# Optimization experiments

Measured on AMD Instinct MI355X. Metric: run time of the kernel, lower is better.

The kernel has to match this reference:

```python
import jax, jax.numpy as jnp
import numpy as np

N = 512
C = 64
B = 1048576


def setup_inputs() -> dict:
    key = jax.random.key(0)
    k1, k2, k3, k4 = jax.random.split(key, 4)
    coords = jax.random.uniform(k1, (B, 3), dtype=jnp.float32, minval=-0.5, maxval=0.5)
    x_line = jax.random.normal(k2, (N, C), dtype=jnp.float32)
    y_line = jax.random.normal(k3, (N, C), dtype=jnp.float32)
    z_line = jax.random.normal(k4, (N, C), dtype=jnp.float32)
    grid = jnp.linspace(-0.5, 0.5, N, dtype=jnp.float32)
    return {"coords": coords, "x_line": x_line, "y_line": y_line, "z_line": z_line, "grid": grid}


def _interp_1d(line_feat, coord, grid):
    # line_feat: [N, C], coord: [B] in [-0.5, 0.5]
    n = line_feat.shape[0]
    pos = (coord - grid[0]) / (grid[1] - grid[0])          # [B] fractional index
    idx0 = jnp.clip(jnp.floor(pos).astype(jnp.int32), 0, n - 2)
    w1 = (pos - idx0.astype(pos.dtype))[:, None]            # [B, 1]
    f0 = line_feat[idx0]                                    # [B, C] gather
    f1 = line_feat[idx0 + 1]                                # [B, C] gather
    return f0 * (1.0 - w1) + f1 * w1


def reference(coords, x_line, y_line, z_line, grid):
    # mode='sum' (default): fx + fy + fz -> [B, C]
    fx = _interp_1d(x_line, coords[:, 0], grid)
    fy = _interp_1d(y_line, coords[:, 1], grid)
    fz = _interp_1d(z_line, coords[:, 2], grid)
    return fx + fy + fz
```

## Files before the change

### kernel.cpp

```cpp
#include <hip/hip_runtime.h>


typedef float f4 __attribute__((ext_vector_type(4)));

constexpr int kN       = 512;
constexpr int kC4      = 16;
constexpr int kGroups  = 4;
constexpr int kPr      = 128;
constexpr int kRowF    = 20;
constexpr int kThreads = 1024;

__global__ __launch_bounds__(kThreads) void triline_lds_kernel(
    const float* __restrict__ coords,
    const f4* __restrict__ xl,
    const f4* __restrict__ yl,
    const f4* __restrict__ zl,
    const float* __restrict__ grid,
    f4* __restrict__ out,
    int B)
{
    __shared__ float sm[3 * kN * kRowF];

    const int bid = blockIdx.x;
    const int g   = bid / kPr;
    const int pr  = bid % kPr;

    for (int i = threadIdx.x; i < kN * 4; i += kThreads) {
        const int r   = i >> 2;
        const int k   = i & 3;
        const int dst = r * kRowF + k * 4;
        const int src = r * kC4 + g * 4 + k;
        *(f4*)&sm[dst]                  = xl[src];
        *(f4*)&sm[kN * kRowF + dst]     = yl[src];
        *(f4*)&sm[2 * kN * kRowF + dst] = zl[src];
    }
    __syncthreads();

    const float g0     = grid[0];
    const float inv_dg = 1.0f / (grid[1] - g0);

    const int p = threadIdx.x >> 2;
    const int k = threadIdx.x & 3;

    const int per  = (B + kPr - 1) / kPr;
    const int b0   = pr * per;
    const int bend = min(b0 + per, B);

    const float* sx = sm;
    const float* sy = sm + kN * kRowF;
    const float* sz = sm + 2 * kN * kRowF;

    int   b  = b0 + p;
    float cx = 0.0f, cy = 0.0f, cz = 0.0f;
    if (b < bend) {
        cx = coords[3 * b + 0];
        cy = coords[3 * b + 1];
        cz = coords[3 * b + 2];
    }

    while (b < bend) {
        const int bn = b + 256;
        float nx = 0.0f, ny = 0.0f, nz = 0.0f;
        if (bn < bend) {
            nx = coords[3 * bn + 0];
            ny = coords[3 * bn + 1];
            nz = coords[3 * bn + 2];
        }

        const float px = (cx - g0) * inv_dg;
        const float py = (cy - g0) * inv_dg;
        const float pz = (cz - g0) * inv_dg;

        const int ix = min(max((int)floorf(px), 0), kN - 2);
        const int iy = min(max((int)floorf(py), 0), kN - 2);
        const int iz = min(max((int)floorf(pz), 0), kN - 2);

        const float wx = px - (float)ix;
        const float wy = py - (float)iy;
        const float wz = pz - (float)iz;

        const f4 x0 = *(const f4*)&sx[ix * kRowF + k * 4];
        const f4 x1 = *(const f4*)&sx[ix * kRowF + kRowF + k * 4];
        const f4 y0 = *(const f4*)&sy[iy * kRowF + k * 4];
        const f4 y1 = *(const f4*)&sy[iy * kRowF + kRowF + k * 4];
        const f4 z0 = *(const f4*)&sz[iz * kRowF + k * 4];
        const f4 z1 = *(const f4*)&sz[iz * kRowF + kRowF + k * 4];

        f4 r = x0 + (x1 - x0) * wx;
        r    = r + y0 + (y1 - y0) * wy;
        r    = r + z0 + (z1 - z0) * wz;

        __builtin_nontemporal_store(r, &out[b * kC4 + g * 4 + k]);

        b  = bn;
        cx = nx; cy = ny; cz = nz;
    }
}

extern "C" void kernel_launch(void* const* d_in, const int* in_sizes, int n_in,
                              void* d_out, int out_size, void* d_ws, size_t ws_size,
                              hipStream_t stream) {
    const float* coords = (const float*)d_in[0];
    const f4*    xl     = (const f4*)d_in[1];
    const f4*    yl     = (const f4*)d_in[2];
    const f4*    zl     = (const f4*)d_in[3];
    const float* grid   = (const float*)d_in[4];
    f4*          out    = (f4*)d_out;

    int B = in_sizes[0] / 3;

    triline_lds_kernel<<<kGroups * kPr, kThreads, 0, stream>>>(
        coords, xl, yl, zl, grid, out, B);
}
```

Before: 318.0 us.

## Software-pipeline two interleaved points per thread and halve grid size

Restructures the main loop so each thread handles two interleaved point streams (A and B). The LDS gathers for one stream are issued while the other stream's results are computed and stored, and coordinates are prefetched two slabs ahead, to hide LDS and global latency. It also halves the number of blocks per channel group, removes the tail bounds checks by assuming B divides evenly, adds a launch-bounds occupancy hint, and replaces the nontemporal stores with regular stores. The exact-division assumption holds for the test size, but the kernel would silently skip points for other sizes.

```diff
diff --git a/kernel.cpp b/kernel.cpp
--- a/kernel.cpp
+++ b/kernel.cpp
@@ -6,11 +6,12 @@
 constexpr int kN       = 512;
 constexpr int kC4      = 16;
 constexpr int kGroups  = 4;
-constexpr int kPr      = 128;
+constexpr int kPr      = 64;
 constexpr int kRowF    = 20;
 constexpr int kThreads = 1024;
+constexpr int kSlab    = 256;
 
-__global__ __launch_bounds__(kThreads) void triline_lds_kernel(
+__global__ __launch_bounds__(kThreads, 4) void triline_v3(
     const float* __restrict__ coords,
     const f4* __restrict__ xl,
     const f4* __restrict__ yl,
@@ -27,9 +28,9 @@
 
     for (int i = threadIdx.x; i < kN * 4; i += kThreads) {
         const int r   = i >> 2;
-        const int k   = i & 3;
-        const int dst = r * kRowF + k * 4;
-        const int src = r * kC4 + g * 4 + k;
+        const int kk  = i & 3;
+        const int dst = r * kRowF + kk * 4;
+        const int src = r * kC4 + g * 4 + kk;
         *(f4*)&sm[dst]                  = xl[src];
         *(f4*)&sm[kN * kRowF + dst]     = yl[src];
         *(f4*)&sm[2 * kN * kRowF + dst] = zl[src];
@@ -39,61 +40,96 @@
     const float g0     = grid[0];
     const float inv_dg = 1.0f / (grid[1] - g0);
 
-    const int p = threadIdx.x >> 2;
-    const int k = threadIdx.x & 3;
+    const int p    = threadIdx.x >> 2;
+    const int kw   = (threadIdx.x & 3) * 4;
+    const int kout = g * 4 + (threadIdx.x & 3);
 
-    const int per  = (B + kPr - 1) / kPr;
+    const int per  = B / kPr;
     const int b0   = pr * per;
-    const int bend = min(b0 + per, B);
+    const int bend = b0 + per;
 
     const float* sx = sm;
     const float* sy = sm + kN * kRowF;
     const float* sz = sm + 2 * kN * kRowF;
 
-    int   b  = b0 + p;
-    float cx = 0.0f, cy = 0.0f, cz = 0.0f;
-    if (b < bend) {
-        cx = coords[3 * b + 0];
-        cy = coords[3 * b + 1];
-        cz = coords[3 * b + 2];
-    }
+    int bA = b0 + p;
+    float cxA = coords[3*bA+0], cyA = coords[3*bA+1], czA = coords[3*bA+2];
 
-    while (b < bend) {
-        const int bn = b + 256;
-        float nx = 0.0f, ny = 0.0f, nz = 0.0f;
-        if (bn < bend) {
-            nx = coords[3 * bn + 0];
-            ny = coords[3 * bn + 1];
-            nz = coords[3 * bn + 2];
-        }
+    float pxA = (cxA - g0) * inv_dg;
+    float pyA = (cyA - g0) * inv_dg;
+    float pzA = (czA - g0) * inv_dg;
+    int ixA = min(max((int)floorf(pxA), 0), kN - 2);
+    int iyA = min(max((int)floorf(pyA), 0), kN - 2);
+    int izA = min(max((int)floorf(pzA), 0), kN - 2);
+    float wxA = pxA - (float)ixA;
+    float wyA = pyA - (float)iyA;
+    float wzA = pzA - (float)izA;
+    f4 Ax0 = *(const f4*)&sx[ixA * kRowF + kw];
+    f4 Ax1 = *(const f4*)&sx[ixA * kRowF + kRowF + kw];
+    f4 Ay0 = *(const f4*)&sy[iyA * kRowF + kw];
+    f4 Ay1 = *(const f4*)&sy[iyA * kRowF + kRowF + kw];
+    f4 Az0 = *(const f4*)&sz[izA * kRowF + kw];
+    f4 Az1 = *(const f4*)&sz[izA * kRowF + kRowF + kw];
 
-        const float px = (cx - g0) * inv_dg;
-        const float py = (cy - g0) * inv_dg;
-        const float pz = (cz - g0) * inv_dg;
+    int bB = bA + kSlab;
+    int bBs = min(bB, bend - 1);
+    float cxB = coords[3*bBs+0], cyB = coords[3*bBs+1], czB = coords[3*bBs+2];
 
-        const int ix = min(max((int)floorf(px), 0), kN - 2);
-        const int iy = min(max((int)floorf(py), 0), kN - 2);
-        const int iz = min(max((int)floorf(pz), 0), kN - 2);
+    const int nIter = per / kSlab;
+    for (int t = 0; t < nIter; t += 2) {
+        float pxB = (cxB - g0) * inv_dg;
+        float pyB = (cyB - g0) * inv_dg;
+        float pzB = (czB - g0) * inv_dg;
+        int ixB = min(max((int)floorf(pxB), 0), kN - 2);
+        int iyB = min(max((int)floorf(pyB), 0), kN - 2);
+        int izB = min(max((int)floorf(pzB), 0), kN - 2);
+        float wxB = pxB - (float)ixB;
+        float wyB = pyB - (float)iyB;
+        float wzB = pzB - (float)izB;
+        f4 Bx0 = *(const f4*)&sx[ixB * kRowF + kw];
+        f4 Bx1 = *(const f4*)&sx[ixB * kRowF + kRowF + kw];
+        f4 By0 = *(const f4*)&sy[iyB * kRowF + kw];
+        f4 By1 = *(const f4*)&sy[iyB * kRowF + kRowF + kw];
+        f4 Bz0 = *(const f4*)&sz[izB * kRowF + kw];
+        f4 Bz1 = *(const f4*)&sz[izB * kRowF + kRowF + kw];
 
-        const float wx = px - (float)ix;
-        const float wy = py - (float)iy;
-        const float wz = pz - (float)iz;
+        const int bN1  = bA + 2 * kSlab;
+        const int bN1s = min(bN1, bend - 1);
+        float cxN = coords[3*bN1s+0], cyN = coords[3*bN1s+1], czN = coords[3*bN1s+2];
 
-        const f4 x0 = *(const f4*)&sx[ix * kRowF + k * 4];
-        const f4 x1 = *(const f4*)&sx[ix * kRowF + kRowF + k * 4];
-        const f4 y0 = *(const f4*)&sy[iy * kRowF + k * 4];
-        const f4 y1 = *(const f4*)&sy[iy * kRowF + kRowF + k * 4];
-        const f4 z0 = *(const f4*)&sz[iz * kRowF + k * 4];
-        const f4 z1 = *(const f4*)&sz[iz * kRowF + kRowF + k * 4];
+        f4 rA = Ax0 + (Ax1 - Ax0) * wxA;
+        rA    = rA + Ay0 + (Ay1 - Ay0) * wyA;
+        rA    = rA + Az0 + (Az1 - Az0) * wzA;
+        out[bA * kC4 + kout] = rA;
 
-        f4 r = x0 + (x1 - x0) * wx;
-        r    = r + y0 + (y1 - y0) * wy;
-        r    = r + z0 + (z1 - z0) * wz;
+        bA = bN1;
+        float pxA2 = (cxN - g0) * inv_dg;
+        float pyA2 = (cyN - g0) * inv_dg;
+        float pzA2 = (czN - g0) * inv_dg;
+        int ixA2 = min(max((int)floorf(pxA2), 0), kN - 2);
+        int iyA2 = min(max((int)floorf(pyA2), 0), kN - 2);
+        int izA2 = min(max((int)floorf(pzA2), 0), kN - 2);
+        wxA = pxA2 - (float)ixA2;
+        wyA = pyA2 - (float)iyA2;
+        wzA = pzA2 - (float)izA2;
+        Ax0 = *(const f4*)&sx[ixA2 * kRowF + kw];
+        Ax1 = *(const f4*)&sx[ixA2 * kRowF + kRowF + kw];
+        Ay0 = *(const f4*)&sy[iyA2 * kRowF + kw];
+        Ay1 = *(const f4*)&sy[iyA2 * kRowF + kRowF + kw];
+        Az0 = *(const f4*)&sz[izA2 * kRowF + kw];
+        Az1 = *(const f4*)&sz[izA2 * kRowF + kRowF + kw];
 
-        __builtin_nontemporal_store(r, &out[b * kC4 + g * 4 + k]);
+        const int bN2  = bB + 2 * kSlab;
+        const int bN2s = min(bN2, bend - 1);
+        cxB = coords[3*bN2s+0];
+        cyB = coords[3*bN2s+1];
+        czB = coords[3*bN2s+2];
 
-        b  = bn;
-        cx = nx; cy = ny; cz = nz;
+        f4 rB = Bx0 + (Bx1 - Bx0) * wxB;
+        rB    = rB + By0 + (By1 - By0) * wyB;
+        rB    = rB + Bz0 + (Bz1 - Bz0) * wzB;
+        out[bB * kC4 + kout] = rB;
+        bB = bN2;
     }
 }
 
@@ -109,6 +145,6 @@
 
     int B = in_sizes[0] / 3;
 
-    triline_lds_kernel<<<kGroups * kPr, kThreads, 0, stream>>>(
+    triline_v3<<<kGroups * kPr, kThreads, 0, stream>>>(
         coords, xl, yl, zl, grid, out, B);
 }
```

Measured after the change: 326.3 us. +2.6%, slower.

## Store line tables in fp16 LDS and interpolate with packed half math

Applied to the files above, without the earlier changes.

Converts the three line-feature tables to fp16 in shared memory and does the lerp-and-sum in packed half precision, with each thread handling 8 channels instead of 4. It doubles the number of blocks and removes the tail bounds handling, assuming B divides evenly into slabs. This reduces LDS footprint and bandwidth and the number of load and arithmetic instructions. In exchange it loses precision versus the fp32 reference and breaks for sizes that do not divide evenly.

```diff
diff --git a/kernel.cpp b/kernel.cpp
--- a/kernel.cpp
+++ b/kernel.cpp
@@ -1,16 +1,18 @@
 #include <hip/hip_runtime.h>
 
 
-typedef float f4 __attribute__((ext_vector_type(4)));
+typedef float    f4 __attribute__((ext_vector_type(4)));
+typedef _Float16 h8 __attribute__((ext_vector_type(8)));
 
 constexpr int kN       = 512;
 constexpr int kC4      = 16;
-constexpr int kGroups  = 4;
-constexpr int kPr      = 128;
-constexpr int kRowF    = 20;
+constexpr int kPr      = 256;
+constexpr int kRowH    = 24;
+constexpr int kTabH    = kN * kRowH;
 constexpr int kThreads = 1024;
+constexpr int kSlab    = 512;
 
-__global__ __launch_bounds__(kThreads) void triline_lds_kernel(
+__global__ __launch_bounds__(kThreads, 8) void triline_v5(
     const float* __restrict__ coords,
     const f4* __restrict__ xl,
     const f4* __restrict__ yl,
@@ -19,53 +21,44 @@
     f4* __restrict__ out,
     int B)
 {
-    __shared__ float sm[3 * kN * kRowF];
+    __shared__ _Float16 sm[3 * kTabH];
 
     const int bid = blockIdx.x;
-    const int g   = bid / kPr;
-    const int pr  = bid % kPr;
+    const int g   = bid >> 8;
+    const int pr  = bid & 255;
 
-    for (int i = threadIdx.x; i < kN * 4; i += kThreads) {
-        const int r   = i >> 2;
-        const int k   = i & 3;
-        const int dst = r * kRowF + k * 4;
-        const int src = r * kC4 + g * 4 + k;
-        *(f4*)&sm[dst]                  = xl[src];
-        *(f4*)&sm[kN * kRowF + dst]     = yl[src];
-        *(f4*)&sm[2 * kN * kRowF + dst] = zl[src];
+    for (int i = threadIdx.x; i < 3 * kN; i += kThreads) {
+        const int tb = i >> 9;
+        const int r  = i & 511;
+        const f4* src = (tb == 0) ? xl : (tb == 1) ? yl : zl;
+        const int sb  = r * kC4 + g * 4;
+        const f4 a0 = src[sb + 0], a1 = src[sb + 1];
+        const f4 a2 = src[sb + 2], a3 = src[sb + 3];
+        h8 lo, hi;
+        lo[0]=(_Float16)a0.x; lo[1]=(_Float16)a0.y; lo[2]=(_Float16)a0.z; lo[3]=(_Float16)a0.w;
+        lo[4]=(_Float16)a1.x; lo[5]=(_Float16)a1.y; lo[6]=(_Float16)a1.z; lo[7]=(_Float16)a1.w;
+        hi[0]=(_Float16)a2.x; hi[1]=(_Float16)a2.y; hi[2]=(_Float16)a2.z; hi[3]=(_Float16)a2.w;
+        hi[4]=(_Float16)a3.x; hi[5]=(_Float16)a3.y; hi[6]=(_Float16)a3.z; hi[7]=(_Float16)a3.w;
+        _Float16* dst = &sm[tb * kTabH + r * kRowH];
+        *(h8*)&dst[0] = lo;
+        *(h8*)&dst[8] = hi;
     }
     __syncthreads();
 
     const float g0     = grid[0];
     const float inv_dg = 1.0f / (grid[1] - g0);
 
-    const int p = threadIdx.x >> 2;
-    const int k = threadIdx.x & 3;
+    const int p  = threadIdx.x >> 1;
+    const int kh = (threadIdx.x & 1) * 8;
+    const int co = g * 4 + (threadIdx.x & 1) * 2;
 
-    const int per  = (B + kPr - 1) / kPr;
-    const int b0   = pr * per;
-    const int bend = min(b0 + per, B);
+    const int b0 = pr * (B / kPr);
 
-    const float* sx = sm;
-    const float* sy = sm + kN * kRowF;
-    const float* sz = sm + 2 * kN * kRowF;
-
-    int   b  = b0 + p;
-    float cx = 0.0f, cy = 0.0f, cz = 0.0f;
-    if (b < bend) {
-        cx = coords[3 * b + 0];
-        cy = coords[3 * b + 1];
-        cz = coords[3 * b + 2];
-    }
-
-    while (b < bend) {
-        const int bn = b + 256;
-        float nx = 0.0f, ny = 0.0f, nz = 0.0f;
-        if (bn < bend) {
-            nx = coords[3 * bn + 0];
-            ny = coords[3 * bn + 1];
-            nz = coords[3 * bn + 2];
-        }
+    for (int t = 0; t < (B / kPr) / kSlab; ++t) {
+        const int b  = b0 + t * kSlab + p;
+        const float cx = coords[3 * b + 0];
+        const float cy = coords[3 * b + 1];
+        const float cz = coords[3 * b + 2];
 
         const float px = (cx - g0) * inv_dg;
         const float py = (cy - g0) * inv_dg;
@@ -75,25 +68,26 @@
         const int iy = min(max((int)floorf(py), 0), kN - 2);
         const int iz = min(max((int)floorf(pz), 0), kN - 2);
 
-        const float wx = px - (float)ix;
-        const float wy = py - (float)iy;
-        const float wz = pz - (float)iz;
+        const _Float16 wx = (_Float16)(px - (float)ix);
+        const _Float16 wy = (_Float16)(py - (float)iy);
+        const _Float16 wz = (_Float16)(pz - (float)iz);
 
-        const f4 x0 = *(const f4*)&sx[ix * kRowF + k * 4];
-        const f4 x1 = *(const f4*)&sx[ix * kRowF + kRowF + k * 4];
-        const f4 y0 = *(const f4*)&sy[iy * kRowF + k * 4];
-        const f4 y1 = *(const f4*)&sy[iy * kRowF + kRowF + k * 4];
-        const f4 z0 = *(const f4*)&sz[iz * kRowF + k * 4];
-        const f4 z1 = *(const f4*)&sz[iz * kRowF + kRowF + k * 4];
+        const h8 x0 = *(const h8*)&sm[ix * kRowH + kh];
+        const h8 x1 = *(const h8*)&sm[ix * kRowH + kRowH + kh];
+        const h8 y0 = *(const h8*)&sm[kTabH + iy * kRowH + kh];
+        const h8 y1 = *(const h8*)&sm[kTabH + iy * kRowH + kRowH + kh];
+        const h8 z0 = *(const h8*)&sm[2 * kTabH + iz * kRowH + kh];
+        const h8 z1 = *(const h8*)&sm[2 * kTabH + iz * kRowH + kRowH + kh];
 
-        f4 r = x0 + (x1 - x0) * wx;
-        r    = r + y0 + (y1 - y0) * wy;
-        r    = r + z0 + (z1 - z0) * wz;
+        h8 acc = x0 + (x1 - x0) * wx;
+        acc    = acc + y0 + (y1 - y0) * wy;
+        acc    = acc + z0 + (z1 - z0) * wz;
 
-        __builtin_nontemporal_store(r, &out[b * kC4 + g * 4 + k]);
+        f4 o0 = { (float)acc[0], (float)acc[1], (float)acc[2], (float)acc[3] };
+        f4 o1 = { (float)acc[4], (float)acc[5], (float)acc[6], (float)acc[7] };
 
-        b  = bn;
-        cx = nx; cy = ny; cz = nz;
+        out[b * kC4 + co]     = o0;
+        out[b * kC4 + co + 1] = o1;
     }
 }
 
@@ -109,6 +103,6 @@
 
     int B = in_sizes[0] / 3;
 
-    triline_lds_kernel<<<kGroups * kPr, kThreads, 0, stream>>>(
+    triline_v5<<<4 * kPr, kThreads, 0, stream>>>(
         coords, xl, yl, zl, grid, out, B);
 }
```

Result: slower. 351.8 us (+10.6%).
